# Performance work log

Measured on AMD Instinct MI355X. Metric: run time of the kernel, lower is better.

## Reference

```python
import jax, jax.numpy as jnp
import numpy as np

EPS = 1e-6
SCALE = 1.0
GRID_HEIGHT = 4.0
GRID_RES_Y = 1.0


def _perspective(mat, vec):
    # mat [3,4], vec [...,3] -> (points [...,2], flag [...,3])
    homog = jnp.einsum('ij,...j->...i', mat[:, :3], vec) + mat[:, 3]
    pos = homog[..., 2:3] > 0
    flag = jnp.concatenate([pos, pos, jnp.ones_like(pos)], axis=-1).astype(homog.dtype)
    homog = homog * flag  # zero x,y behind camera; z kept (flag[...,-1]=True)
    return homog[..., :2] / homog[..., 2:3], flag


def _fisheye(pts, k, D, flag):
    cx, cy, fx, fy = k[0, 2], k[1, 2], k[0, 0], k[1, 1]
    x = (pts[..., 0] - cx) / fx
    y = (pts[..., 1] - cy) / fy
    r = jnp.sqrt(x * x + y * y)
    th = jnp.arctan(r)
    t2 = th * th
    rad = th * (1 + D[0] * t2 + D[1] * t2 ** 2 + D[2] * t2 ** 3 + D[5] * t2 ** 4) / r
    xd = x * rad * fx + cx
    yd = y * rad * fy + cy
    return jnp.stack([xd, yd], axis=-1) * flag[..., :2]


def _pinhole(pts, k, D, flag):
    cx, cy, fx, fy = k[0, 2], k[1, 2], k[0, 0], k[1, 1]
    x = (pts[..., 0] - cx) / fx
    y = (pts[..., 1] - cy) / fy
    k1, k2, k3, p1, p2 = D[0], D[1], D[2], D[3], D[4]
    r2 = x * x + y * y
    poly = 1 + k1 * r2 + k2 * r2 * r2 + k3 * r2 * r2 * r2
    xd = x * poly + (2 * p1 * x * y + p2 * (r2 + 2 * x * x))
    yd = y * poly + (p1 * (r2 + 2 * y * y) + 2 * p2 * x * y)
    return jnp.stack([xd * fx + cx, yd * fy + cy], axis=-1) * flag[..., :2]


def _bilinear(img, coords):
    # torch F.grid_sample(align_corners=True, padding_mode='border'); img [C,H,W], coords [...,2] in [-1,1]
    C, H, W = img.shape
    x = jnp.clip((coords[..., 0] + 1) * 0.5 * (W - 1), 0.0, W - 1)
    y = jnp.clip((coords[..., 1] + 1) * 0.5 * (H - 1), 0.0, H - 1)
    x0 = jnp.floor(x)
    y0 = jnp.floor(y)
    wx = x - x0
    wy = y - y0
    x0i = x0.astype(jnp.int32)
    y0i = y0.astype(jnp.int32)
    x1i = jnp.minimum(x0i + 1, W - 1)
    y1i = jnp.minimum(y0i + 1, H - 1)
    flat = img.reshape(C, H * W)

    def g(yi, xi):
        return jnp.take(flat, (yi * W + xi).reshape(-1), axis=1).reshape((C,) + coords.shape[:-1])

    v00 = g(y0i, x0i)
    v01 = g(y0i, x1i)
    v10 = g(y1i, x0i)
    v11 = g(y1i, x1i)
    return v00 * (1 - wx) * (1 - wy) + v01 * wx * (1 - wy) + v10 * (1 - wx) * wy + v11 * wx * wy


def _per_image(feature, k, imu2c, post_rot, post_tran, undist, corner):
    C, Hf, Wf = feature.shape
    calib = k @ imu2c                                  # [3,4]
    pts, flag = _perspective(calib, corner)            # pts [Ny,Zd,Xd,2]
    pts = jnp.where(undist[-1] == 1,
                    _fisheye(pts, k, undist, flag),
                    _pinhole(pts, k, undist, flag))
    pts = jnp.einsum('ij,...j->...i', post_rot[:2, :2], pts) + post_tran[:2]
    nc = jnp.clip(2.0 * (pts / SCALE) - 1.0, -1.0, 1.0)  # [Ny,Zd,Xd,2]
    s0, s1 = slice(None, -1), slice(1, None)
    # 8 voxel corners -> [8, Ny-1, D, Wd, 2]
    corners8 = jnp.stack([nc[a, b, c] for a in (s0, s1) for b in (s0, s1) for c in (s0, s1)], axis=0)
    left = corners8[..., 0].min(0)
    right = corners8[..., 0].max(0)
    top = corners8[..., 1].min(0)
    bot = corners8[..., 1].max(0)
    Nh, D, Wd = left.shape
    bbox = jnp.stack([left, top, right, bot], axis=-1).reshape(Nh, D * Wd, 4)
    area = (bbox[..., 2] - bbox[..., 0]) * (bbox[..., 3] - bbox[..., 1]) * Hf * Wf * 0.25 + EPS  # [Nh,P]
    integ = jnp.cumsum(jnp.cumsum(feature, axis=-1), axis=-2)  # integral image [C,Hf,Wf]
    tl = _bilinear(integ, bbox[..., 0:2])
    br = _bilinear(integ, bbox[..., 2:4])
    tr = _bilinear(integ, jnp.stack([bbox[..., 2], bbox[..., 1]], axis=-1))
    bl = _bilinear(integ, jnp.stack([bbox[..., 0], bbox[..., 3]], axis=-1))
    vox = (tl + br - tr - bl) / area * (area > EPS)    # [C,Nh,P]
    return vox.reshape(C * Nh, D, Wd)                  # neck == '2d'


def _forward(features, ks, imu2cs, post_rots, post_trans, undists, grid):
    ys = -jnp.arange(0.0, GRID_HEIGHT, GRID_RES_Y) + GRID_HEIGHT / 2.0
    y_corners = jnp.stack([jnp.zeros_like(ys), ys, jnp.zeros_like(ys)], axis=-1)  # [Ny,3]
    corners = grid[:, None] + y_corners[None, :, None, None, :]                   # [B,Ny,Zd,Xd,3]
    per_cam = jax.vmap(_per_image, in_axes=(0, 0, 0, 0, 0, 0, None))

    def per_batch(f, k, m, pr, pt, ud, c):
        # drop_idx = [] -> all cameras kept; max over cameras
        return per_cam(f, k, m, pr, pt, ud, c).max(axis=0)

    return jax.vmap(per_batch)(features, ks, imu2cs, post_rots, post_trans, undists, corners)


def setup_inputs():
    key = jax.random.key(0)
    B, N, C, Hf, Wf = 1, 6, 64, 64, 176
    Zd = Xd = 129
    kf, ku = jax.random.split(key, 2)
    features = jax.random.normal(kf, (B, N, C, Hf, Wf), jnp.float32)
    # intrinsics (realistic pinhole values keep the projection numerically sane)
    K = np.zeros((B, N, 3, 3), np.float32)
    K[..., 0, 0] = 600.0
    K[..., 1, 1] = 600.0
    K[..., 0, 2] = 704.0
    K[..., 1, 2] = 256.0
    K[..., 2, 2] = 1.0
    ks = jnp.asarray(K)
    # extrinsics: per-camera yaw + small translation
    m = np.zeros((B, N, 3, 4), np.float32)
    for i in range(N):
        th = 0.25 * (i - 2.5)
        R = np.array([[np.cos(th), 0.0, np.sin(th)],
                      [0.0, 1.0, 0.0],
                      [-np.sin(th), 0.0, np.cos(th)]], np.float32)
        m[:, i, :, :3] = R
        m[:, i, :, 3] = np.array([0.1 * i, -1.5, 0.2], np.float32)
    imu2cs = jnp.asarray(m)
    pr = np.zeros((B, N, 3, 3), np.float32)
    pr[..., 0, 0] = 1.0 / 1408.0
    pr[..., 1, 1] = 1.0 / 512.0
    pr[..., 2, 2] = 1.0
    post_rots = jnp.asarray(pr)
    post_trans = jnp.zeros((B, N, 3), jnp.float32)
    und = 0.01 * np.array(jax.random.normal(ku, (B, N, 7)), np.float32)
    und[..., 6] = 0.0
    und[:, :3, 6] = 1.0  # first 3 cameras fisheye, rest pinhole
    undists = jnp.asarray(und)
    x = np.linspace(-40.0, 40.0, Xd, dtype=np.float32)
    z = np.linspace(3.0, 80.0, Zd, dtype=np.float32)
    zz, xx = np.meshgrid(z, x, indexing='ij')
    g = np.stack([xx, np.zeros_like(xx), zz], axis=-1)[None]  # [1,Zd,Xd,3]
    grid = jnp.asarray(np.broadcast_to(g, (B, Zd, Xd, 3)).copy())
    return {"features": features, "ks": ks, "imu2cs": imu2cs, "post_rots": post_rots,
            "post_trans": post_trans, "undists": undists, "grid": grid}


def reference(features, ks, imu2cs, post_rots, post_trans, undists, grid):
    return _forward(features, ks, imu2cs, post_rots, post_trans, undists, grid)
```

## Files before the change

### kernel.cpp

```cpp
#include <hip/hip_runtime.h>
#include <math.h>

#define NCAM 6
#define C_CH 64
#define HF   64
#define WF   176
#define GDIM 129
#define NY   4
#define NH   3
#define DD   128
#define WDIM 128
#define NP   (DD*WDIM)

struct alignas(16) BoxP {
    int   oTL, oTR, oBL, oBR;
    float wxL, wxR, wyT, wyB;
    float area;
    int   pad0, pad1, pad2;
};
static_assert(sizeof(BoxP) == 48, "BoxP size");

__device__ __forceinline__ int rfl_i(int x) {
    return __builtin_amdgcn_readfirstlane(x);
}
__device__ __forceinline__ float rfl_f(float x) {
    return __builtin_bit_cast(float, __builtin_amdgcn_readfirstlane(__builtin_bit_cast(int, x)));
}

__global__ __launch_bounds__(256) void k_rowcum(const float* __restrict__ feat,
                                                float* __restrict__ rowsum)
{
    __shared__ float T[WF * 65];
    __shared__ float S[4][C_CH];
    __shared__ float OFF[4][C_CH];
    const int h   = blockIdx.x;
    const int n   = blockIdx.y;
    const int tid = threadIdx.x;

    for (int idx = tid; idx < C_CH * WF; idx += 256) {
        const int cc = idx / WF;
        const int w  = idx % WF;
        T[w*65 + cc] = feat[((size_t)(n*C_CH + cc)*HF + h)*WF + w];
    }
    __syncthreads();
    {
        const int cc = tid & 63, seg = tid >> 6;
        const int w0 = seg * 44;
        float run = 0.0f;
        #pragma unroll
        for (int i = 0; i < 44; ++i) {
            run += T[(w0 + i)*65 + cc];
            T[(w0 + i)*65 + cc] = run;
        }
        S[seg][cc] = run;
    }
    __syncthreads();
    {
        const int cc = tid & 63, seg = tid >> 6;
        float off = 0.0f;
        #pragma unroll
        for (int s = 0; s < 3; ++s)
            if (s < seg) off += S[s][cc];
        OFF[seg][cc] = off;
    }
    __syncthreads();
    float* outp = rowsum + (size_t)(n*HF + h) * (WF * C_CH);
    for (int idx = tid; idx < WF * C_CH; idx += 256) {
        const int w  = idx >> 6;
        const int cc = idx & 63;
        outp[idx] = T[w*65 + cc] + OFF[w/44][cc];
    }
}

__global__ __launch_bounds__(256) void k_quadcol(const float* __restrict__ rowsum,
                                                 float4* __restrict__ qbuf)
{
    __shared__ float tA[4][C_CH], tB[4][C_CH];
    __shared__ float fA[4][C_CH], fB[4][C_CH];
    const int x  = blockIdx.x;
    const int n  = blockIdx.y;
    const int x1 = min(x + 1, WF - 1);
    const int c  = threadIdx.x & 63;
    const int hq = threadIdx.x >> 6;

    const float* base0 = rowsum + (size_t)n*HF*WF*C_CH + (size_t)x  * C_CH + c;
    const float* base1 = rowsum + (size_t)n*HF*WF*C_CH + (size_t)x1 * C_CH + c;

    float eA[16], eB[16];
    #pragma unroll
    for (int i = 0; i < 16; ++i) {
        const int h = hq*16 + i;
        eA[i] = base0[(size_t)h * (WF*C_CH)];
        eB[i] = base1[(size_t)h * (WF*C_CH)];
    }
    float sA[16], sB[16];
    sA[0] = eA[0]; sB[0] = eB[0];
    #pragma unroll
    for (int i = 1; i < 16; ++i) {
        sA[i] = sA[i-1] + eA[i];
        sB[i] = sB[i-1] + eB[i];
    }
    tA[hq][c] = sA[15]; tB[hq][c] = sB[15];
    fA[hq][c] = eA[0];  fB[hq][c] = eB[0];
    __syncthreads();

    float offA = 0.0f, offB = 0.0f;
    #pragma unroll
    for (int s = 0; s < 3; ++s)
        if (s < hq) { offA += tA[s][c]; offB += tB[s][c]; }

    float nextA, nextB;
    if (hq < 3) {
        nextA = fA[hq+1][c] + (offA + tA[hq][c]);
        nextB = fB[hq+1][c] + (offB + tB[hq][c]);
    } else {
        nextA = sA[15] + offA;
        nextB = sB[15] + offB;
    }

    float4* qb = qbuf + ((size_t)n*HF*WF + x) * C_CH + c;
    #pragma unroll
    for (int i = 0; i < 16; ++i) {
        const int h = hq*16 + i;
        float4 q;
        q.x = sA[i] + offA;
        q.y = sB[i] + offB;
        if (i < 15) {
            q.z = sA[i+1] + offA;
            q.w = sB[i+1] + offB;
        } else {
            q.z = nextA;
            q.w = nextB;
        }
        qb[(size_t)h * (WF*C_CH)] = q;
    }
}

__global__ void k_boxproj(const float* __restrict__ ks,
                          const float* __restrict__ imu2cs,
                          const float* __restrict__ post_rots,
                          const float* __restrict__ post_trans,
                          const float* __restrict__ undists,
                          const float* __restrict__ grid,
                          BoxP* __restrict__ bp)
{
    const int idx = blockIdx.x * blockDim.x + threadIdx.x;
    if (idx >= NCAM * NH * NP) return;
    const int n  = idx / (NH * NP);
    const int r  = idx % (NH * NP);
    const int nh = r / NP;
    const int p  = r % NP;
    const int d  = p / WDIM;
    const int wd = p % WDIM;

    const float* k  = ks         + n * 9;
    const float* m  = imu2cs     + n * 12;
    const float* pr = post_rots  + n * 9;
    const float* pt = post_trans + n * 3;
    const float* D  = undists    + n * 7;

    float cal[12];
    #pragma unroll
    for (int i = 0; i < 3; ++i)
        #pragma unroll
        for (int j = 0; j < 4; ++j)
            cal[i*4+j] = k[i*3+0]*m[0*4+j] + k[i*3+1]*m[1*4+j] + k[i*3+2]*m[2*4+j];

    const float fx = k[0], fy = k[4], cx = k[2], cy = k[5];
    const bool fish = (D[6] == 1.0f);
    const float D0 = D[0], D1 = D[1], D2 = D[2], D3 = D[3], D4 = D[4], D5 = D[5];

    float left = 1e30f, right = -1e30f, top = 1e30f, bot = -1e30f;
    #pragma unroll
    for (int a = 0; a < 2; ++a) {
        const float vy = 2.0f - (float)(nh + a);
        #pragma unroll
        for (int b = 0; b < 2; ++b) {
            #pragma unroll
            for (int cc = 0; cc < 2; ++cc) {
                const int gz = d + b, gx = wd + cc;
                const float vx = grid[(gz*GDIM + gx)*3 + 0];
                const float vz = grid[(gz*GDIM + gx)*3 + 2];

                const float hx = cal[0]*vx + cal[1]*vy + cal[2]*vz  + cal[3];
                const float hy = cal[4]*vx + cal[5]*vy + cal[6]*vz  + cal[7];
                const float hz = cal[8]*vx + cal[9]*vy + cal[10]*vz + cal[11];

                const float fl = (hz > 0.0f) ? 1.0f : 0.0f;
                const float px = (hx * fl) / hz;
                const float py = (hy * fl) / hz;

                const float x = (px - cx) / fx;
                const float y = (py - cy) / fy;

                float xd, yd;
                if (fish) {
                    const float rr = sqrtf(x*x + y*y);
                    const float th = atanf(rr);
                    const float t2 = th * th;
                    const float t4 = t2 * t2;
                    const float rad = th * (1.0f + D0*t2 + D1*t4 + D2*(t2*t4) + D5*(t4*t4)) / rr;
                    xd = x * rad * fx + cx;
                    yd = y * rad * fy + cy;
                } else {
                    const float r2 = x*x + y*y;
                    const float poly = 1.0f + D0*r2 + D1*r2*r2 + D2*r2*r2*r2;
                    const float xdd = x*poly + (2.0f*D3*x*y + D4*(r2 + 2.0f*x*x));
                    const float ydd = y*poly + (D3*(r2 + 2.0f*y*y) + 2.0f*D4*x*y);
                    xd = xdd * fx + cx;
                    yd = ydd * fy + cy;
                }
                xd *= fl; yd *= fl;

                const float qx = pr[0]*xd + pr[1]*yd + pt[0];
                const float qy = pr[3]*xd + pr[4]*yd + pt[1];
                const float ncx = fminf(fmaxf(2.0f*qx - 1.0f, -1.0f), 1.0f);
                const float ncy = fminf(fmaxf(2.0f*qy - 1.0f, -1.0f), 1.0f);

                left  = fminf(left,  ncx);  right = fmaxf(right, ncx);
                top   = fminf(top,   ncy);  bot   = fmaxf(bot,   ncy);
            }
        }
    }

    const float area = (right - left) * (bot - top) * (float)HF * (float)WF * 0.25f + 1e-6f;

    const float xLp = fminf(fmaxf((left  + 1.0f) * 0.5f * (float)(WF-1), 0.0f), (float)(WF-1));
    const float xRp = fminf(fmaxf((right + 1.0f) * 0.5f * (float)(WF-1), 0.0f), (float)(WF-1));
    const float yTp = fminf(fmaxf((top   + 1.0f) * 0.5f * (float)(HF-1), 0.0f), (float)(HF-1));
    const float yBp = fminf(fmaxf((bot   + 1.0f) * 0.5f * (float)(HF-1), 0.0f), (float)(HF-1));
    const float xL0 = floorf(xLp), xR0 = floorf(xRp), yT0 = floorf(yTp), yB0 = floorf(yBp);

    const int rT = (int)yT0 * (WF*C_CH*16);
    const int rB = (int)yB0 * (WF*C_CH*16);
    const int cL = (int)xL0 * (C_CH*16);
    const int cR = (int)xR0 * (C_CH*16);

    BoxP o;
    o.oTL = rT + cL; o.oTR = rT + cR; o.oBL = rB + cL; o.oBR = rB + cR;
    o.wxL = xLp - xL0; o.wxR = xRp - xR0; o.wyT = yTp - yT0; o.wyB = yBp - yB0;
    o.area = area; o.pad0 = 0; o.pad1 = 0; o.pad2 = 0;
    bp[idx] = o;
}

__global__ __launch_bounds__(256) void k_sample(const float4* __restrict__ qbuf,
                                                const BoxP* __restrict__ bp,
                                                float* __restrict__ out)
{
    __shared__ float sm[C_CH][33];
    const int nh   = blockIdx.y;
    const int p0   = blockIdx.x * 32;
    const int tid  = threadIdx.x;
    const int wave = __builtin_amdgcn_readfirstlane(tid >> 6);
    const int c    = tid & 63;

    #pragma unroll 1
    for (int j = 0; j < 8; ++j) {
        const int pj = p0 + wave*8 + j;
        const BoxP* bb = bp + nh*NP + pj;
        float vmax = -3.402823466e38f;
        #pragma unroll
        for (int n = 0; n < NCAM; ++n) {
            const BoxP* bpp = bb + n * (NH*NP);
            const float area = rfl_f(bpp->area);
            const int oTL = rfl_i(bpp->oTL), oTR = rfl_i(bpp->oTR);
            const int oBL = rfl_i(bpp->oBL), oBR = rfl_i(bpp->oBR);
            const float wxL = rfl_f(bpp->wxL), wxR = rfl_f(bpp->wxR);
            const float wyT = rfl_f(bpp->wyT), wyB = rfl_f(bpp->wyB);

            const char* qb = (const char*)qbuf + (size_t)n * ((size_t)HF*WF*C_CH*16);
            const float4 qTL = ((const float4*)(qb + (size_t)oTL))[c];
            const float4 qTR = ((const float4*)(qb + (size_t)oTR))[c];
            const float4 qBL = ((const float4*)(qb + (size_t)oBL))[c];
            const float4 qBR = ((const float4*)(qb + (size_t)oBR))[c];

            auto BIL = [&](const float4& q, float wx, float wy) -> float {
                const float m0 = fmaf(wx, q.y - q.x, q.x);
                const float m1 = fmaf(wx, q.w - q.z, q.z);
                return fmaf(wy, m1 - m0, m0);
            };
            const float tl = BIL(qTL, wxL, wyT);
            const float tr = BIL(qTR, wxR, wyT);
            const float bl = BIL(qBL, wxL, wyB);
            const float br = BIL(qBR, wxR, wyB);
            const float s  = (tl + br) - (tr + bl);
            float v = s * __builtin_amdgcn_rcpf(area);
            v = (area > 1e-6f) ? v : 0.0f;
            vmax = fmaxf(vmax, v);
        }
        sm[c][wave*8 + j] = vmax;
    }
    __syncthreads();
    for (int idx = tid; idx < C_CH * 32; idx += 256) {
        const int cc = idx >> 5;
        const int jj = idx & 31;
        out[(size_t)(cc*NH + nh)*NP + p0 + jj] = sm[cc][jj];
    }
}

extern "C" void kernel_launch(void* const* d_in, const int* in_sizes, int n_in,
                              void* d_out, int out_size, void* d_ws, size_t ws_size,
                              hipStream_t stream)
{
    const float* feats      = (const float*)d_in[0];
    const float* ks         = (const float*)d_in[1];
    const float* imu2cs     = (const float*)d_in[2];
    const float* post_rots  = (const float*)d_in[3];
    const float* post_trans = (const float*)d_in[4];
    const float* undists    = (const float*)d_in[5];
    const float* grid       = (const float*)d_in[6];
    float* out = (float*)d_out;

    char* ws = (char*)d_ws;
    size_t off = 0;
    float* rowsum = (float*)(ws + off);
    off += sizeof(float) * NCAM * HF * WF * C_CH;
    off = (off + 255) & ~(size_t)255;
    float4* qbuf = (float4*)(ws + off);
    off += sizeof(float4) * (size_t)NCAM * HF * WF * C_CH;
    off = (off + 255) & ~(size_t)255;
    BoxP* bp = (BoxP*)(ws + off);
    off += sizeof(BoxP) * NCAM * NH * NP;
    (void)ws_size; (void)in_sizes; (void)n_in; (void)out_size;

    dim3 g1(HF, NCAM);
    k_rowcum<<<g1, 256, 0, stream>>>(feats, rowsum);

    dim3 g2(WF, NCAM);
    k_quadcol<<<g2, 256, 0, stream>>>(rowsum, qbuf);

    dim3 g3((NCAM*NH*NP + 255)/256);
    k_boxproj<<<g3, 256, 0, stream>>>(ks, imu2cs, post_rots, post_trans, undists, grid, bp);

    dim3 g4(NP/32, NH);
    k_sample<<<g4, 256, 0, stream>>>(qbuf, bp, out);
}
```

Measured before the change: 162.6 us.

## Replace quad-packed integral buffer with plain integral image and split-corner sampling

Drops the 4x-replicated float4 quad buffer and keeps a plain summed-area table. The column-cumsum kernel writes a quarter of the data. The sampler now has each 16-lane group load one corner column's float4 across 4 channels, combining bilinear weights algebraically and reducing with cross-lane shuffles. It also software-pipelines the next camera's loads and tiles output as 4x8 (d,w) blocks. This cuts workspace traffic and the size of the gather footprint, in exchange for extra shuffles and a larger BoxP record.

```diff
diff --git a/kernel.cpp b/kernel.cpp
--- a/kernel.cpp
+++ b/kernel.cpp
@@ -12,13 +12,18 @@
 #define WDIM 128
 #define NP   (DD*WDIM)
 
+#define ROWB (WF*C_CH*4)
+#define COLB (C_CH*4)
+#define IMGB ((size_t)HF*WF*C_CH*4)
+
 struct alignas(16) BoxP {
-    int   oTL, oTR, oBL, oBR;
+    int   r0, r1, r2, r3;
+    int   c0, c1, c2, c3;
     float wxL, wxR, wyT, wyB;
     float area;
     int   pad0, pad1, pad2;
 };
-static_assert(sizeof(BoxP) == 48, "BoxP size");
+static_assert(sizeof(BoxP) == 64, "BoxP size");
 
 __device__ __forceinline__ int rfl_i(int x) {
     return __builtin_amdgcn_readfirstlane(x);
@@ -72,68 +77,33 @@
     }
 }
 
-__global__ __launch_bounds__(256) void k_quadcol(const float* __restrict__ rowsum,
-                                                 float4* __restrict__ qbuf)
-{
-    __shared__ float tA[4][C_CH], tB[4][C_CH];
-    __shared__ float fA[4][C_CH], fB[4][C_CH];
+__global__ __launch_bounds__(256) void k_colcum(const float* __restrict__ rowsum,
+                                                float* __restrict__ integ)
+{
+    __shared__ float tA[4][C_CH];
     const int x  = blockIdx.x;
     const int n  = blockIdx.y;
-    const int x1 = min(x + 1, WF - 1);
     const int c  = threadIdx.x & 63;
     const int hq = threadIdx.x >> 6;
 
-    const float* base0 = rowsum + (size_t)n*HF*WF*C_CH + (size_t)x  * C_CH + c;
-    const float* base1 = rowsum + (size_t)n*HF*WF*C_CH + (size_t)x1 * C_CH + c;
-
-    float eA[16], eB[16];
-    #pragma unroll
-    for (int i = 0; i < 16; ++i) {
-        const int h = hq*16 + i;
-        eA[i] = base0[(size_t)h * (WF*C_CH)];
-        eB[i] = base1[(size_t)h * (WF*C_CH)];
-    }
-    float sA[16], sB[16];
-    sA[0] = eA[0]; sB[0] = eB[0];
-    #pragma unroll
-    for (int i = 1; i < 16; ++i) {
-        sA[i] = sA[i-1] + eA[i];
-        sB[i] = sB[i-1] + eB[i];
-    }
-    tA[hq][c] = sA[15]; tB[hq][c] = sB[15];
-    fA[hq][c] = eA[0];  fB[hq][c] = eB[0];
-    __syncthreads();
-
-    float offA = 0.0f, offB = 0.0f;
+    const float* base = rowsum + (size_t)n*HF*WF*C_CH + (size_t)x * C_CH + c;
+    float e[16];
+    #pragma unroll
+    for (int i = 0; i < 16; ++i)
+        e[i] = base[(size_t)(hq*16 + i) * (WF*C_CH)];
+    #pragma unroll
+    for (int i = 1; i < 16; ++i)
+        e[i] += e[i-1];
+    tA[hq][c] = e[15];
+    __syncthreads();
+    float off = 0.0f;
     #pragma unroll
     for (int s = 0; s < 3; ++s)
-        if (s < hq) { offA += tA[s][c]; offB += tB[s][c]; }
-
-    float nextA, nextB;
-    if (hq < 3) {
-        nextA = fA[hq+1][c] + (offA + tA[hq][c]);
-        nextB = fB[hq+1][c] + (offB + tB[hq][c]);
-    } else {
-        nextA = sA[15] + offA;
-        nextB = sB[15] + offB;
-    }
-
-    float4* qb = qbuf + ((size_t)n*HF*WF + x) * C_CH + c;
-    #pragma unroll
-    for (int i = 0; i < 16; ++i) {
-        const int h = hq*16 + i;
-        float4 q;
-        q.x = sA[i] + offA;
-        q.y = sB[i] + offB;
-        if (i < 15) {
-            q.z = sA[i+1] + offA;
-            q.w = sB[i+1] + offB;
-        } else {
-            q.z = nextA;
-            q.w = nextB;
-        }
-        qb[(size_t)h * (WF*C_CH)] = q;
-    }
+        if (s < hq) off += tA[s][c];
+    float* outp = integ + (size_t)n*HF*WF*C_CH + (size_t)x * C_CH + c;
+    #pragma unroll
+    for (int i = 0; i < 16; ++i)
+        outp[(size_t)(hq*16 + i) * (WF*C_CH)] = e[i] + off;
 }
 
 __global__ void k_boxproj(const float* __restrict__ ks,
@@ -231,70 +201,105 @@
     const float yBp = fminf(fmaxf((bot   + 1.0f) * 0.5f * (float)(HF-1), 0.0f), (float)(HF-1));
     const float xL0 = floorf(xLp), xR0 = floorf(xRp), yT0 = floorf(yTp), yB0 = floorf(yBp);
 
-    const int rT = (int)yT0 * (WF*C_CH*16);
-    const int rB = (int)yB0 * (WF*C_CH*16);
-    const int cL = (int)xL0 * (C_CH*16);
-    const int cR = (int)xR0 * (C_CH*16);
+    const int ixL0 = (int)xL0, ixR0 = (int)xR0, iyT0 = (int)yT0, iyB0 = (int)yB0;
+    const int ixL1 = min(ixL0 + 1, WF-1), ixR1 = min(ixR0 + 1, WF-1);
+    const int iyT1 = min(iyT0 + 1, HF-1), iyB1 = min(iyB0 + 1, HF-1);
 
     BoxP o;
-    o.oTL = rT + cL; o.oTR = rT + cR; o.oBL = rB + cL; o.oBR = rB + cR;
+    o.r0 = iyT0 * ROWB; o.r1 = iyT1 * ROWB; o.r2 = iyB0 * ROWB; o.r3 = iyB1 * ROWB;
+    o.c0 = ixL0 * COLB; o.c1 = ixL1 * COLB; o.c2 = ixR0 * COLB; o.c3 = ixR1 * COLB;
     o.wxL = xLp - xL0; o.wxR = xRp - xR0; o.wyT = yTp - yT0; o.wyB = yBp - yB0;
     o.area = area; o.pad0 = 0; o.pad1 = 0; o.pad2 = 0;
     bp[idx] = o;
 }
 
-__global__ __launch_bounds__(256) void k_sample(const float4* __restrict__ qbuf,
+__global__ __launch_bounds__(256) void k_sample(const float* __restrict__ integ,
                                                 const BoxP* __restrict__ bp,
                                                 float* __restrict__ out)
 {
-    __shared__ float sm[C_CH][33];
+    __shared__ float sm[32][68];
     const int nh   = blockIdx.y;
-    const int p0   = blockIdx.x * 32;
+    const int t    = blockIdx.x;
+    const int d0   = (t >> 4) * 4;
+    const int w0   = (t & 15) * 8;
     const int tid  = threadIdx.x;
     const int wave = __builtin_amdgcn_readfirstlane(tid >> 6);
-    const int c    = tid & 63;
+    const int lane = tid & 63;
+    const int g    = lane >> 4;
+    const int q    = lane & 15;
+    const int qoff = q * 16;
+    const int d    = d0 + wave;
+
+    auto ISSUE = [&](int cam, int pv,
+                     float4& v0, float4& v1, float4& v2, float4& v3,
+                     float& vg, float& wT, float& wB, float& ar) {
+        const BoxP* bb = bp + ((cam*NH + nh)*NP + pv);
+        ar = rfl_f(bb->area);
+        const int r0 = rfl_i(bb->r0), r1 = rfl_i(bb->r1);
+        const int r2 = rfl_i(bb->r2), r3 = rfl_i(bb->r3);
+        const int c0 = rfl_i(bb->c0), c1 = rfl_i(bb->c1);
+        const int c2 = rfl_i(bb->c2), c3 = rfl_i(bb->c3);
+        const float wxL = rfl_f(bb->wxL), wxR = rfl_f(bb->wxR);
+        wT = rfl_f(bb->wyT); wB = rfl_f(bb->wyB);
+        const int co = (g == 0) ? c0 : (g == 1) ? c1 : (g == 2) ? c2 : c3;
+        vg = (g == 0) ? (1.0f - wxL) : (g == 1) ? wxL
+           : (g == 2) ? (wxR - 1.0f) : -wxR;
+        const char* base = (const char*)integ + (size_t)cam * IMGB + (size_t)(co + qoff);
+        v0 = *(const float4*)(base + r0);
+        v1 = *(const float4*)(base + r1);
+        v2 = *(const float4*)(base + r2);
+        v3 = *(const float4*)(base + r3);
+    };
+
+    const int pbase = d * WDIM + w0;
+    float4 a0, a1, a2, a3; float avg, awT, awB, aar;
+    ISSUE(0, pbase, a0, a1, a2, a3, avg, awT, awB, aar);
 
     #pragma unroll 1
     for (int j = 0; j < 8; ++j) {
-        const int pj = p0 + wave*8 + j;
-        const BoxP* bb = bp + nh*NP + pj;
-        float vmax = -3.402823466e38f;
+        const int pj = pbase + j;
+        float4 vm = make_float4(-3.402823466e38f, -3.402823466e38f,
+                                -3.402823466e38f, -3.402823466e38f);
         #pragma unroll
         for (int n = 0; n < NCAM; ++n) {
-            const BoxP* bpp = bb + n * (NH*NP);
-            const float area = rfl_f(bpp->area);
-            const int oTL = rfl_i(bpp->oTL), oTR = rfl_i(bpp->oTR);
-            const int oBL = rfl_i(bpp->oBL), oBR = rfl_i(bpp->oBR);
-            const float wxL = rfl_f(bpp->wxL), wxR = rfl_f(bpp->wxR);
-            const float wyT = rfl_f(bpp->wyT), wyB = rfl_f(bpp->wyB);
-
-            const char* qb = (const char*)qbuf + (size_t)n * ((size_t)HF*WF*C_CH*16);
-            const float4 qTL = ((const float4*)(qb + (size_t)oTL))[c];
-            const float4 qTR = ((const float4*)(qb + (size_t)oTR))[c];
-            const float4 qBL = ((const float4*)(qb + (size_t)oBL))[c];
-            const float4 qBR = ((const float4*)(qb + (size_t)oBR))[c];
-
-            auto BIL = [&](const float4& q, float wx, float wy) -> float {
-                const float m0 = fmaf(wx, q.y - q.x, q.x);
-                const float m1 = fmaf(wx, q.w - q.z, q.z);
-                return fmaf(wy, m1 - m0, m0);
-            };
-            const float tl = BIL(qTL, wxL, wyT);
-            const float tr = BIL(qTR, wxR, wyT);
-            const float bl = BIL(qBL, wxL, wyB);
-            const float br = BIL(qBR, wxR, wyB);
-            const float s  = (tl + br) - (tr + bl);
-            float v = s * __builtin_amdgcn_rcpf(area);
-            v = (area > 1e-6f) ? v : 0.0f;
-            vmax = fmaxf(vmax, v);
+            float4 b0, b1, b2, b3; float bvg, bwT, bwB, bar;
+            if (n < 5) {
+                ISSUE(n+1, pj, b0, b1, b2, b3, bvg, bwT, bwB, bar);
+            } else if (j < 7) {
+                ISSUE(0, pj+1, b0, b1, b2, b3, bvg, bwT, bwB, bar);
+            } else {
+                b0 = a0; b1 = a1; b2 = a2; b3 = a3;
+                bvg = avg; bwT = awT; bwB = awB; bar = aar;
+            }
+            const float u0 = 1.0f - awT, u1 = awT, u2 = awB - 1.0f, u3 = -awB;
+            float px = fmaf(u0, a0.x, fmaf(u1, a1.x, fmaf(u2, a2.x, u3*a3.x))) * avg;
+            float py = fmaf(u0, a0.y, fmaf(u1, a1.y, fmaf(u2, a2.y, u3*a3.y))) * avg;
+            float pz = fmaf(u0, a0.z, fmaf(u1, a1.z, fmaf(u2, a2.z, u3*a3.z))) * avg;
+            float pw = fmaf(u0, a0.w, fmaf(u1, a1.w, fmaf(u2, a2.w, u3*a3.w))) * avg;
+            px += __shfl_xor(px, 16, 64); px += __shfl_xor(px, 32, 64);
+            py += __shfl_xor(py, 16, 64); py += __shfl_xor(py, 32, 64);
+            pz += __shfl_xor(pz, 16, 64); pz += __shfl_xor(pz, 32, 64);
+            pw += __shfl_xor(pw, 16, 64); pw += __shfl_xor(pw, 32, 64);
+            const float ia = __builtin_amdgcn_rcpf(aar);
+            const bool ok = (aar > 1e-6f);
+            vm.x = fmaxf(vm.x, ok ? px*ia : 0.0f);
+            vm.y = fmaxf(vm.y, ok ? py*ia : 0.0f);
+            vm.z = fmaxf(vm.z, ok ? pz*ia : 0.0f);
+            vm.w = fmaxf(vm.w, ok ? pw*ia : 0.0f);
+            a0 = b0; a1 = b1; a2 = b2; a3 = b3;
+            avg = bvg; awT = bwT; awB = bwB; aar = bar;
         }
-        sm[c][wave*8 + j] = vmax;
+        if (g == 0) {
+            *(float4*)&sm[wave*8 + j][4*q] = vm;
+        }
     }
     __syncthreads();
     for (int idx = tid; idx < C_CH * 32; idx += 256) {
+        const int jj = idx & 31;
         const int cc = idx >> 5;
-        const int jj = idx & 31;
-        out[(size_t)(cc*NH + nh)*NP + p0 + jj] = sm[cc][jj];
+        const int dd = d0 + (jj >> 3);
+        const int ww = w0 + (jj & 7);
+        out[(size_t)(cc*NH + nh)*NP + dd*WDIM + ww] = sm[jj][cc];
     }
 }
 
@@ -314,24 +319,24 @@
     char* ws = (char*)d_ws;
     size_t off = 0;
     float* rowsum = (float*)(ws + off);
-    off += sizeof(float) * NCAM * HF * WF * C_CH;
+    off += sizeof(float) * (size_t)NCAM * HF * WF * C_CH;
     off = (off + 255) & ~(size_t)255;
-    float4* qbuf = (float4*)(ws + off);
-    off += sizeof(float4) * (size_t)NCAM * HF * WF * C_CH;
+    float* integ = (float*)(ws + off);
+    off += sizeof(float) * (size_t)NCAM * HF * WF * C_CH;
     off = (off + 255) & ~(size_t)255;
     BoxP* bp = (BoxP*)(ws + off);
-    off += sizeof(BoxP) * NCAM * NH * NP;
+    off += sizeof(BoxP) * (size_t)NCAM * NH * NP;
     (void)ws_size; (void)in_sizes; (void)n_in; (void)out_size;
 
     dim3 g1(HF, NCAM);
     k_rowcum<<<g1, 256, 0, stream>>>(feats, rowsum);
 
     dim3 g2(WF, NCAM);
-    k_quadcol<<<g2, 256, 0, stream>>>(rowsum, qbuf);
+    k_colcum<<<g2, 256, 0, stream>>>(rowsum, integ);
 
     dim3 g3((NCAM*NH*NP + 255)/256);
     k_boxproj<<<g3, 256, 0, stream>>>(ks, imu2cs, post_rots, post_trans, undists, grid, bp);
 
-    dim3 g4(NP/32, NH);
-    k_sample<<<g4, 256, 0, stream>>>(qbuf, bp, out);
-}
+    dim3 g4(512, NH);
+    k_sample<<<g4, 256, 0, stream>>>(integ, bp, out);
+}
```

Result: slower. 169.9 us (+4.5%).
